# Performance work log

Hardware: AMD Instinct MI355X
Metric: run time of the kernel (lower is better)

Reference implementation:

```python
import jax, jax.numpy as jnp
import numpy as np

EMBED_DIM = 1024
NUM_HEADS = 16
HEAD_DIM = EMBED_DIM // NUM_HEADS
BSZ, TGT, SRC = 4, 1024, 2048


def setup_inputs() -> dict:
    key = jax.random.key(0)
    ks = jax.random.split(key, 12)
    init = 1.0 / np.sqrt(EMBED_DIM)
    return {
        "hidden_states": jax.random.normal(ks[0], (BSZ, TGT, EMBED_DIM), jnp.float32),
        "key_value_states": jax.random.normal(ks[1], (BSZ, SRC, EMBED_DIM), jnp.float32),
        "bias": jax.random.normal(ks[2], (BSZ, NUM_HEADS, TGT, SRC), jnp.float32),
        "Wq": jax.random.normal(ks[3], (EMBED_DIM, EMBED_DIM), jnp.float32) * init,
        "bq": jax.random.normal(ks[4], (EMBED_DIM,), jnp.float32) * init,
        "Wk": jax.random.normal(ks[5], (EMBED_DIM, EMBED_DIM), jnp.float32) * init,
        "bk": jax.random.normal(ks[6], (EMBED_DIM,), jnp.float32) * init,
        "Wv": jax.random.normal(ks[7], (EMBED_DIM, EMBED_DIM), jnp.float32) * init,
        "bv": jax.random.normal(ks[8], (EMBED_DIM,), jnp.float32) * init,
        "Wo": jax.random.normal(ks[9], (EMBED_DIM, EMBED_DIM), jnp.float32) * init,
        "bo": jax.random.normal(ks[10], (EMBED_DIM,), jnp.float32) * init,
    }


def reference(hidden_states, key_value_states, bias, Wq, bq, Wk, bk, Wv, bv, Wo, bo):
    B, T, E = hidden_states.shape
    S = key_value_states.shape[1]
    H, hd = NUM_HEADS, HEAD_DIM
    scaling = hd ** (-0.5)
    # torch Linear: y = x @ W^T + b
    q = (hidden_states @ Wq.T + bq) * scaling            # [B,T,E]
    k = key_value_states @ Wk.T + bk                     # [B,S,E]
    v = key_value_states @ Wv.T + bv                     # [B,S,E]
    q = q.reshape(B, T, H, hd).transpose(0, 2, 1, 3)     # [B,H,T,hd]
    k = k.reshape(B, S, H, hd).transpose(0, 2, 1, 3)     # [B,H,S,hd]
    v = v.reshape(B, S, H, hd).transpose(0, 2, 1, 3)     # [B,H,S,hd]
    scores = jnp.einsum('bhtd,bhsd->bhts', q, k) + bias  # [B,H,T,S]
    probs = jax.nn.softmax(scores, axis=-1)
    attn = jnp.einsum('bhts,bhsd->bhtd', probs, v)       # [B,H,T,hd]
    # Faithful to the original: reshape (B*H, T, hd) -> (B, T, E) WITHOUT
    # transposing heads back (this is how the torch source does it).
    attn = attn.reshape(B, T, E)
    return attn @ Wo.T + bo
```

## Files before the change

kernel.cpp:

```cpp
#include <hip/hip_runtime.h>

#define DEVI __device__ __forceinline__

typedef __attribute__((ext_vector_type(4))) float f32x4;
typedef __attribute__((ext_vector_type(8))) short bf16x8;

DEVI unsigned short f2bf(float f) {
  unsigned int u = __builtin_bit_cast(unsigned int, f);
  u += 0x7FFFu + ((u >> 16) & 1u);
  return (unsigned short)(u >> 16);
}

DEVI void load_lds16(const void* g, void* l) {
  __builtin_amdgcn_global_load_lds(
      (__attribute__((address_space(1))) void*)g,
      (__attribute__((address_space(3))) void*)l,
      16, 0, 0);
}

DEVI int xcd_swz(int bid, int chunk) { return (bid & 7) * chunk + (bid >> 3); }

struct CvtArgs {
  const float* src[6];
  unsigned short* dst[6];
  int cum[6];
};

__global__ __launch_bounds__(256) void cvt_all(CvtArgs a, int total4) {
  int i = blockIdx.x * 256 + threadIdx.x;
  if (i >= total4) return;
  int s = 0;
#pragma unroll
  for (int k = 1; k < 6; ++k) s += (i >= a.cum[k]);
  const int j = i - a.cum[s];
  const f32x4 v = __builtin_nontemporal_load((const f32x4*)a.src[s] + j);
  ushort4 o;
  o.x = f2bf(v[0]); o.y = f2bf(v[1]); o.z = f2bf(v[2]); o.w = f2bf(v[3]);
  reinterpret_cast<ushort4*>(a.dst[s])[j] = o;
}

template<bool OUT_BF16>
DEVI void gemm_core(const unsigned short* __restrict__ A,
                    const unsigned short* __restrict__ W,
                    const float* __restrict__ bias,
                    void* __restrict__ out,
                    float scale, int log2R,
                    long sb, long st, long sh, long sd,
                    int bx, int by, bool vt)
{
  constexpr int K = 1024;
  __shared__ unsigned short smem[2 * 128 * 64];
  unsigned short* As = smem;
  unsigned short* Bs = smem + 8192;

  const int tid  = threadIdx.x;
  const int wid  = tid >> 6;
  const int lane = tid & 63;
  const int m0 = bx * 128;
  const int n0 = by * 128;
  const int wr = (wid >> 1) * 64;
  const int wc = (wid & 1) * 64;
  const int lg = lane >> 4;
  const int ll = lane & 15;

  f32x4 acc[4][4] = {};

  const char* Ab = (const char*)A + (long)m0 * K * 2;
  const char* Wb = (const char*)W + (long)n0 * K * 2;
  char* AsB = (char*)As;
  char* BsB = (char*)Bs;
  const long rowstride = (long)K * 2;

  for (int kt = 0; kt < K; kt += 64) {
#pragma unroll
    for (int j = 0; j < 4; ++j) {
      const int o    = (wid * 4 + j) * 1024 + lane * 16;
      const int row  = o >> 7;
      const int colb = o & 127;
      load_lds16(Ab + (long)row * rowstride + (long)kt * 2 + colb, AsB + (wid * 4 + j) * 1024);
      load_lds16(Wb + (long)row * rowstride + (long)kt * 2 + colb, BsB + (wid * 4 + j) * 1024);
    }
    __syncthreads();
#pragma unroll
    for (int ks = 0; ks < 2; ++ks) {
      bf16x8 af[4], bfr[4];
#pragma unroll
      for (int i = 0; i < 4; ++i) {
        af[i]  = *(const bf16x8*)&As[(wr + i * 16 + ll) * 64 + ks * 32 + lg * 8];
        bfr[i] = *(const bf16x8*)&Bs[(wc + i * 16 + ll) * 64 + ks * 32 + lg * 8];
      }
#pragma unroll
      for (int i = 0; i < 4; ++i)
#pragma unroll
        for (int j = 0; j < 4; ++j)
          acc[i][j] = __builtin_amdgcn_mfma_f32_16x16x32_bf16(af[i], bfr[j], acc[i][j], 0, 0, 0);
    }
    __syncthreads();
  }

  const int Rmask  = (1 << log2R) - 1;
  const int m_base = m0 + wr;
  const int b   = m_base >> log2R;
  const int tbs = m_base & Rmask;
  const int nn  = n0 + wc;
  float bj[4];
#pragma unroll
  for (int j = 0; j < 4; ++j) bj[j] = bias[nn + j * 16 + ll];

  if (OUT_BF16 && vt) {
    unsigned short* Tw = smem + wid * 2176;
#pragma unroll
    for (int h2 = 0; h2 < 2; ++h2) {
#pragma unroll
      for (int jj = 0; jj < 2; ++jj) {
        const int j = h2 * 2 + jj;
#pragma unroll
        for (int i = 0; i < 4; ++i)
#pragma unroll
          for (int r = 0; r < 4; ++r)
            Tw[(jj * 16 + ll) * 68 + i * 16 + lg * 4 + r] = f2bf((acc[i][j][r] + bj[j]) * scale);
      }
      asm volatile("s_waitcnt lgkmcnt(0)" ::: "memory");
#pragma unroll
      for (int k = 0; k < 8; ++k) {
        const int dloc = k * 4 + lg;
        const int t4   = ll * 4;
        const ushort4 vv = *(const ushort4*)&Tw[dloc * 68 + t4];
        const int n = nn + h2 * 32 + dloc;
        const int h = n >> 6, dd = n & 63;
        *(ushort4*)((unsigned short*)out + (long)b * sb + (long)h * sh + (long)dd * sd + tbs + t4) = vv;
      }
      if (h2 == 0) asm volatile("s_waitcnt lgkmcnt(0)" ::: "memory");
    }
    return;
  }

  if (OUT_BF16) {
    const int h = nn >> 6;
    unsigned short* ob = (unsigned short*)out + (long)b * sb + (long)h * sh;
    unsigned short* Tw = smem + wid * 2176;
#pragma unroll
    for (int p = 0; p < 2; ++p) {
#pragma unroll
      for (int i2 = 0; i2 < 2; ++i2) {
        const int i = p * 2 + i2;
#pragma unroll
        for (int j = 0; j < 4; ++j)
#pragma unroll
          for (int r = 0; r < 4; ++r)
            Tw[(i2 * 16 + lg * 4 + r) * 68 + j * 16 + ll] = f2bf((acc[i][j][r] + bj[j]) * scale);
      }
      asm volatile("s_waitcnt lgkmcnt(0)" ::: "memory");
#pragma unroll
      for (int k = 0; k < 8; ++k) {
        const int t_loc = k * 4 + lg;
        const int d4    = ll * 4;
        const ushort4 vv = *(const ushort4*)&Tw[t_loc * 68 + d4];
        *(ushort4*)(ob + (long)(tbs + p * 32 + t_loc) * st + d4) = vv;
      }
      if (p == 0) asm volatile("s_waitcnt lgkmcnt(0)" ::: "memory");
    }
    return;
  }

  {
    float* ob = (float*)out + (long)b * sb + nn;
    float* TwF = (float*)smem + wid * 1056;
#pragma unroll
    for (int i = 0; i < 4; ++i) {
#pragma unroll
      for (int j = 0; j < 4; ++j)
#pragma unroll
        for (int r = 0; r < 4; ++r)
          TwF[(lg * 4 + r) * 66 + j * 16 + ll] = acc[i][j][r] + bj[j];
      asm volatile("s_waitcnt lgkmcnt(0)" ::: "memory");
#pragma unroll
      for (int k = 0; k < 8; ++k) {
        const int t_loc = k * 2 + (lane >> 5);
        const int c2    = (lane & 31) * 2;
        const float2 v = *(const float2*)&TwF[t_loc * 66 + c2];
        *(float2*)(ob + (long)(tbs + i * 16 + t_loc) * st + c2) = v;
      }
      if (i < 3) asm volatile("s_waitcnt lgkmcnt(0)" ::: "memory");
    }
  }
}

struct GemmDesc {
  const unsigned short* A;
  const unsigned short* W;
  const float* bias;
  unsigned short* out;
  float scale;
  int log2R;
  long sb, st, sh, sd;
};

__global__ __launch_bounds__(256) void gemm_qkv(GemmDesc d0, GemmDesc d1, GemmDesc d2) {
  int bid = xcd_swz(blockIdx.x, 160);
  const GemmDesc* d;
  bool vt = false;
  if (bid < 256)      { d = &d0; }
  else if (bid < 768) { d = &d1; bid -= 256; }
  else                { d = &d2; bid -= 768; vt = true; }
  gemm_core<true>(d->A, d->W, d->bias, d->out, d->scale, d->log2R,
                  d->sb, d->st, d->sh, d->sd, bid >> 3, bid & 7, vt);
}

__global__ __launch_bounds__(256) void gemm_o(
    const unsigned short* __restrict__ A,
    const unsigned short* __restrict__ W,
    const float* __restrict__ bias,
    float* __restrict__ out,
    long sb, long st, long sh, long sd)
{
  const int bid = xcd_swz(blockIdx.x, 32);
  gemm_core<false>(A, W, bias, out, 1.0f, 10, sb, st, sh, sd, bid >> 3, bid & 7, false);
}

__global__ __launch_bounds__(256, 4) void attn_fused(
    const unsigned short* __restrict__ Qb,
    const unsigned short* __restrict__ Kb,
    const unsigned short* __restrict__ Vt,
    const float* __restrict__ bias,
    unsigned short* __restrict__ Ob)
{
  constexpr int T = 1024, S = 2048;
  __shared__ unsigned short Ks[64 * 72];
  __shared__ unsigned short Vs[64 * 72];
  __shared__ unsigned short Ps[4][16 * 72];

  const int tid = threadIdx.x;
  const int w = tid >> 6, lane = tid & 63;
  const int lg = lane >> 4, ll = lane & 15;

  const int wg = xcd_swz(blockIdx.x, 128);
  const int bh = wg >> 4;
  const int tt = wg & 15;
  const int t0 = tt * 64;
  const int trow = t0 + w * 16;

  bf16x8 qf[2];
#pragma unroll
  for (int ks = 0; ks < 2; ++ks)
    qf[ks] = *(const bf16x8*)(Qb + ((long)bh * T + trow + ll) * 64 + ks * 32 + lg * 8);

  f32x4 acc[4] = {};
  float m_run = -1e30f, l_run = 0.0f;

  const char* Kg = (const char*)(Kb + (long)bh * S * 64);
  const char* Vg = (const char*)(Vt + (long)bh * 64 * S);
  const float* biasg = bias + ((long)bh * T + t0) * S;
  const float* bias_row = biasg + (long)(w * 16 + ll) * S + lg * 4;

  for (int sc = 0; sc < S / 64; ++sc) {
    const float* bp = bias_row + sc * 64;
    f32x4 b4[4];
#pragma unroll
    for (int sf = 0; sf < 4; ++sf)
      b4[sf] = __builtin_nontemporal_load((const f32x4*)(bp + sf * 16));

#pragma unroll
    for (int r2 = 0; r2 < 2; ++r2) {
      const int o = (tid + r2 * 256) * 16;
      const int row = o >> 7, colb = o & 127;
      uint4 kd = *(const uint4*)(Kg + (long)(sc * 64 + row) * 128 + colb);
      *(uint4*)((char*)&Ks[0] + row * 144 + colb) = kd;
      uint4 vd = *(const uint4*)(Vg + (long)row * (S * 2) + sc * 128 + colb);
      *(uint4*)((char*)&Vs[0] + row * 144 + colb) = vd;
    }
    __syncthreads();

    f32x4 sv[4] = {};
#pragma unroll
    for (int ks = 0; ks < 2; ++ks) {
      bf16x8 kf[4];
#pragma unroll
      for (int sf = 0; sf < 4; ++sf)
        kf[sf] = *(const bf16x8*)((const char*)&Ks[0] + (sf * 16 + ll) * 144 + (ks * 32 + lg * 8) * 2);
#pragma unroll
      for (int sf = 0; sf < 4; ++sf)
        sv[sf] = __builtin_amdgcn_mfma_f32_16x16x32_bf16(kf[sf], qf[ks], sv[sf], 0, 0, 0);
    }

#pragma unroll
    for (int sf = 0; sf < 4; ++sf) {
      sv[sf][0] += b4[sf][0]; sv[sf][1] += b4[sf][1];
      sv[sf][2] += b4[sf][2]; sv[sf][3] += b4[sf][3];
    }

    float cm = sv[0][0];
#pragma unroll
    for (int sf = 0; sf < 4; ++sf)
#pragma unroll
      for (int r = 0; r < 4; ++r) cm = fmaxf(cm, sv[sf][r]);
    cm = fmaxf(cm, __shfl_xor(cm, 16));
    cm = fmaxf(cm, __shfl_xor(cm, 32));

    const float mnew = fmaxf(m_run, cm);
    const float alpha = __expf(m_run - mnew);
    float ps = 0.0f;
#pragma unroll
    for (int sf = 0; sf < 4; ++sf)
#pragma unroll
      for (int r = 0; r < 4; ++r) {
        const float p = __expf(sv[sf][r] - mnew);
        sv[sf][r] = p;
        ps += p;
      }
    ps += __shfl_xor(ps, 16);
    ps += __shfl_xor(ps, 32);
    l_run = l_run * alpha + ps;
    m_run = mnew;

    float ar[4];
#pragma unroll
    for (int r = 0; r < 4; ++r) ar[r] = __shfl(alpha, lg * 4 + r);
#pragma unroll
    for (int df = 0; df < 4; ++df)
#pragma unroll
      for (int r = 0; r < 4; ++r) acc[df][r] *= ar[r];

    unsigned short* Pw = &Ps[w][0];
#pragma unroll
    for (int sf = 0; sf < 4; ++sf) {
      ushort4 pw;
      pw.x = f2bf(sv[sf][0]); pw.y = f2bf(sv[sf][1]);
      pw.z = f2bf(sv[sf][2]); pw.w = f2bf(sv[sf][3]);
      *(ushort4*)&Pw[ll * 72 + sf * 16 + lg * 4] = pw;
    }
    asm volatile("s_waitcnt lgkmcnt(0)" ::: "memory");
    __builtin_amdgcn_sched_barrier(0);

#pragma unroll
    for (int ks = 0; ks < 2; ++ks) {
      bf16x8 pa = *(const bf16x8*)((const char*)Pw + ll * 144 + ks * 64 + lg * 16);
      bf16x8 vf[4];
#pragma unroll
      for (int df = 0; df < 4; ++df)
        vf[df] = *(const bf16x8*)((const char*)&Vs[0] + (df * 16 + ll) * 144 + (ks * 32 + lg * 8) * 2);
#pragma unroll
      for (int df = 0; df < 4; ++df)
        acc[df] = __builtin_amdgcn_mfma_f32_16x16x32_bf16(pa, vf[df], acc[df], 0, 0, 0);
    }
    __syncthreads();
  }

  const float inv = 1.0f / l_run;
  float ir[4];
#pragma unroll
  for (int r = 0; r < 4; ++r) ir[r] = __shfl(inv, lg * 4 + r);
#pragma unroll
  for (int df = 0; df < 4; ++df)
#pragma unroll
    for (int r = 0; r < 4; ++r) {
      const long oo = ((long)bh * T + trow + lg * 4 + r) * 64 + df * 16 + ll;
      Ob[oo] = f2bf(acc[df][r] * ir[r]);
    }
}

extern "C" void kernel_launch(void* const* d_in, const int* in_sizes, int n_in,
                              void* d_out, int out_size, void* d_ws, size_t ws_size,
                              hipStream_t stream) {
  constexpr int B = 4, T = 1024, S = 2048, E = 1024;
  const float* hs   = (const float*)d_in[0];
  const float* kv   = (const float*)d_in[1];
  const float* bias = (const float*)d_in[2];
  const float* Wq   = (const float*)d_in[3];
  const float* bq   = (const float*)d_in[4];
  const float* Wk   = (const float*)d_in[5];
  const float* bk   = (const float*)d_in[6];
  const float* Wv   = (const float*)d_in[7];
  const float* bv   = (const float*)d_in[8];
  const float* Wo   = (const float*)d_in[9];
  const float* bo   = (const float*)d_in[10];

  char* ws = (char*)d_ws;
  const size_t MB = 1024 * 1024;
  unsigned short* hs_bf = (unsigned short*)(ws);
  unsigned short* kv_bf = (unsigned short*)(ws + 8 * MB);
  unsigned short* wq_bf = (unsigned short*)(ws + 24 * MB);
  unsigned short* wk_bf = (unsigned short*)(ws + 26 * MB);
  unsigned short* wv_bf = (unsigned short*)(ws + 28 * MB);
  unsigned short* wo_bf = (unsigned short*)(ws + 30 * MB);
  unsigned short* q_buf = (unsigned short*)(ws + 32 * MB);
  unsigned short* k_buf = (unsigned short*)(ws + 40 * MB);
  unsigned short* v_buf = (unsigned short*)(ws + 56 * MB);
  unsigned short* a_buf = (unsigned short*)(ws + 72 * MB);

  CvtArgs ca;
  ca.src[0] = hs;  ca.dst[0] = hs_bf;
  ca.src[1] = kv;  ca.dst[1] = kv_bf;
  ca.src[2] = Wq;  ca.dst[2] = wq_bf;
  ca.src[3] = Wk;  ca.dst[3] = wk_bf;
  ca.src[4] = Wv;  ca.dst[4] = wv_bf;
  ca.src[5] = Wo;  ca.dst[5] = wo_bf;
  const int n4_hs = B * T * E / 4, n4_kv = B * S * E / 4, n4_w = E * E / 4;
  ca.cum[0] = 0;
  ca.cum[1] = n4_hs;
  ca.cum[2] = n4_hs + n4_kv;
  ca.cum[3] = n4_hs + n4_kv + n4_w;
  ca.cum[4] = n4_hs + n4_kv + 2 * n4_w;
  ca.cum[5] = n4_hs + n4_kv + 3 * n4_w;
  const int total4 = n4_hs + n4_kv + 4 * n4_w;
  cvt_all<<<dim3((total4 + 255) / 256), dim3(256), 0, stream>>>(ca, total4);

  GemmDesc dq{hs_bf, wq_bf, bq, q_buf, 0.125f, 10,
              (long)T * E, 64L, (long)T * 64, 1L};
  GemmDesc dk{kv_bf, wk_bf, bk, k_buf, 1.0f, 11,
              (long)S * E, 64L, (long)S * 64, 1L};
  GemmDesc dv{kv_bf, wv_bf, bv, v_buf, 1.0f, 11,
              (long)S * E, 1L, (long)S * 64, (long)S};
  gemm_qkv<<<dim3(1280), 256, 0, stream>>>(dq, dk, dv);

  attn_fused<<<dim3(1024), 256, 0, stream>>>(q_buf, k_buf, v_buf, bias, a_buf);

  gemm_o<<<dim3(256), 256, 0, stream>>>(
      a_buf, wo_bf, bo, (float*)d_out,
      (long)T * E, (long)E, 64L, 1L);
}
```

Before: 277.3 us.

## Double query rows per wave in attention and prefetch K/V into registers

```diff
diff --git a/kernel.cpp b/kernel.cpp
--- a/kernel.cpp
+++ b/kernel.cpp
@@ -218,7 +218,7 @@
   gemm_core<false>(A, W, bias, out, 1.0f, 10, sb, st, sh, sd, bid >> 3, bid & 7, false);
 }
 
-__global__ __launch_bounds__(256, 4) void attn_fused(
+__global__ __launch_bounds__(256, 2) void attn_fused(
     const unsigned short* __restrict__ Qb,
     const unsigned short* __restrict__ Kb,
     const unsigned short* __restrict__ Vt,
@@ -228,50 +228,64 @@
   constexpr int T = 1024, S = 2048;
   __shared__ unsigned short Ks[64 * 72];
   __shared__ unsigned short Vs[64 * 72];
-  __shared__ unsigned short Ps[4][16 * 72];
+  __shared__ unsigned short Ps[4][32 * 72];
 
   const int tid = threadIdx.x;
   const int w = tid >> 6, lane = tid & 63;
   const int lg = lane >> 4, ll = lane & 15;
 
-  const int wg = xcd_swz(blockIdx.x, 128);
-  const int bh = wg >> 4;
-  const int tt = wg & 15;
-  const int t0 = tt * 64;
-  const int trow = t0 + w * 16;
-
-  bf16x8 qf[2];
-#pragma unroll
-  for (int ks = 0; ks < 2; ++ks)
-    qf[ks] = *(const bf16x8*)(Qb + ((long)bh * T + trow + ll) * 64 + ks * 32 + lg * 8);
-
-  f32x4 acc[4] = {};
-  float m_run = -1e30f, l_run = 0.0f;
+  const int wg = xcd_swz(blockIdx.x, 64);
+  const int bh = wg >> 3;
+  const int tt = wg & 7;
+  const int t0 = tt * 128;
+  const int trow = t0 + w * 32;
+
+  bf16x8 qf[2][2];
+#pragma unroll
+  for (int rf = 0; rf < 2; ++rf)
+#pragma unroll
+    for (int ks = 0; ks < 2; ++ks)
+      qf[rf][ks] = *(const bf16x8*)(Qb + ((long)bh * T + trow + rf * 16 + ll) * 64 + ks * 32 + lg * 8);
+
+  f32x4 acc[2][4] = {};
+  float m_run[2] = {-1e30f, -1e30f};
+  float l_run[2] = {0.0f, 0.0f};
 
   const char* Kg = (const char*)(Kb + (long)bh * S * 64);
   const char* Vg = (const char*)(Vt + (long)bh * 64 * S);
-  const float* biasg = bias + ((long)bh * T + t0) * S;
-  const float* bias_row = biasg + (long)(w * 16 + ll) * S + lg * 4;
+  const float* bias_base = bias + ((long)bh * T + trow + ll) * S + lg * 4;
+
+  const int o0 = tid * 16;
+  const int row0 = o0 >> 7, colb0 = o0 & 127;
+  const int o1 = (tid + 256) * 16;
+  const int row1 = o1 >> 7, colb1 = o1 & 127;
+  uint4 kreg[2], vreg[2];
+  auto load_chunk = [&](int sc) {
+    kreg[0] = *(const uint4*)(Kg + (long)(sc * 64 + row0) * 128 + colb0);
+    vreg[0] = *(const uint4*)(Vg + (long)row0 * (S * 2) + sc * 128 + colb0);
+    kreg[1] = *(const uint4*)(Kg + (long)(sc * 64 + row1) * 128 + colb1);
+    vreg[1] = *(const uint4*)(Vg + (long)row1 * (S * 2) + sc * 128 + colb1);
+  };
+  load_chunk(0);
 
   for (int sc = 0; sc < S / 64; ++sc) {
-    const float* bp = bias_row + sc * 64;
-    f32x4 b4[4];
-#pragma unroll
-    for (int sf = 0; sf < 4; ++sf)
-      b4[sf] = __builtin_nontemporal_load((const f32x4*)(bp + sf * 16));
-
-#pragma unroll
-    for (int r2 = 0; r2 < 2; ++r2) {
-      const int o = (tid + r2 * 256) * 16;
-      const int row = o >> 7, colb = o & 127;
-      uint4 kd = *(const uint4*)(Kg + (long)(sc * 64 + row) * 128 + colb);
-      *(uint4*)((char*)&Ks[0] + row * 144 + colb) = kd;
-      uint4 vd = *(const uint4*)(Vg + (long)row * (S * 2) + sc * 128 + colb);
-      *(uint4*)((char*)&Vs[0] + row * 144 + colb) = vd;
-    }
+    const float* bp = bias_base + sc * 64;
+    f32x4 b4[2][4];
+#pragma unroll
+    for (int rf = 0; rf < 2; ++rf)
+#pragma unroll
+      for (int sf = 0; sf < 4; ++sf)
+        b4[rf][sf] = __builtin_nontemporal_load((const f32x4*)(bp + (long)(rf * 16) * S + sf * 16));
+
+    *(uint4*)((char*)&Ks[0] + row0 * 144 + colb0) = kreg[0];
+    *(uint4*)((char*)&Vs[0] + row0 * 144 + colb0) = vreg[0];
+    *(uint4*)((char*)&Ks[0] + row1 * 144 + colb1) = kreg[1];
+    *(uint4*)((char*)&Vs[0] + row1 * 144 + colb1) = vreg[1];
+
+    if (sc + 1 < S / 64) load_chunk(sc + 1);
     __syncthreads();
 
-    f32x4 sv[4] = {};
+    f32x4 sv[2][4] = {};
 #pragma unroll
     for (int ks = 0; ks < 2; ++ks) {
       bf16x8 kf[4];
@@ -279,84 +293,95 @@
       for (int sf = 0; sf < 4; ++sf)
         kf[sf] = *(const bf16x8*)((const char*)&Ks[0] + (sf * 16 + ll) * 144 + (ks * 32 + lg * 8) * 2);
 #pragma unroll
+      for (int rf = 0; rf < 2; ++rf)
+#pragma unroll
+        for (int sf = 0; sf < 4; ++sf)
+          sv[rf][sf] = __builtin_amdgcn_mfma_f32_16x16x32_bf16(kf[sf], qf[rf][ks], sv[rf][sf], 0, 0, 0);
+    }
+
+    unsigned short* Pw = &Ps[w][0];
+#pragma unroll
+    for (int rf = 0; rf < 2; ++rf) {
+#pragma unroll
+      for (int sf = 0; sf < 4; ++sf) {
+        sv[rf][sf][0] += b4[rf][sf][0]; sv[rf][sf][1] += b4[rf][sf][1];
+        sv[rf][sf][2] += b4[rf][sf][2]; sv[rf][sf][3] += b4[rf][sf][3];
+      }
+      float cm = sv[rf][0][0];
+#pragma unroll
       for (int sf = 0; sf < 4; ++sf)
-        sv[sf] = __builtin_amdgcn_mfma_f32_16x16x32_bf16(kf[sf], qf[ks], sv[sf], 0, 0, 0);
-    }
-
-#pragma unroll
-    for (int sf = 0; sf < 4; ++sf) {
-      sv[sf][0] += b4[sf][0]; sv[sf][1] += b4[sf][1];
-      sv[sf][2] += b4[sf][2]; sv[sf][3] += b4[sf][3];
-    }
-
-    float cm = sv[0][0];
-#pragma unroll
-    for (int sf = 0; sf < 4; ++sf)
-#pragma unroll
-      for (int r = 0; r < 4; ++r) cm = fmaxf(cm, sv[sf][r]);
-    cm = fmaxf(cm, __shfl_xor(cm, 16));
-    cm = fmaxf(cm, __shfl_xor(cm, 32));
-
-    const float mnew = fmaxf(m_run, cm);
-    const float alpha = __expf(m_run - mnew);
-    float ps = 0.0f;
-#pragma unroll
-    for (int sf = 0; sf < 4; ++sf)
-#pragma unroll
-      for (int r = 0; r < 4; ++r) {
-        const float p = __expf(sv[sf][r] - mnew);
-        sv[sf][r] = p;
-        ps += p;
-      }
-    ps += __shfl_xor(ps, 16);
-    ps += __shfl_xor(ps, 32);
-    l_run = l_run * alpha + ps;
-    m_run = mnew;
-
-    float ar[4];
-#pragma unroll
-    for (int r = 0; r < 4; ++r) ar[r] = __shfl(alpha, lg * 4 + r);
-#pragma unroll
-    for (int df = 0; df < 4; ++df)
-#pragma unroll
-      for (int r = 0; r < 4; ++r) acc[df][r] *= ar[r];
-
-    unsigned short* Pw = &Ps[w][0];
-#pragma unroll
-    for (int sf = 0; sf < 4; ++sf) {
-      ushort4 pw;
-      pw.x = f2bf(sv[sf][0]); pw.y = f2bf(sv[sf][1]);
-      pw.z = f2bf(sv[sf][2]); pw.w = f2bf(sv[sf][3]);
-      *(ushort4*)&Pw[ll * 72 + sf * 16 + lg * 4] = pw;
+#pragma unroll
+        for (int r = 0; r < 4; ++r) cm = fmaxf(cm, sv[rf][sf][r]);
+      cm = fmaxf(cm, __shfl_xor(cm, 16));
+      cm = fmaxf(cm, __shfl_xor(cm, 32));
+
+      const float mnew = fmaxf(m_run[rf], cm);
+      const float alpha = __expf(m_run[rf] - mnew);
+      float ps = 0.0f;
+#pragma unroll
+      for (int sf = 0; sf < 4; ++sf)
+#pragma unroll
+        for (int r = 0; r < 4; ++r) {
+          const float p = __expf(sv[rf][sf][r] - mnew);
+          sv[rf][sf][r] = p;
+          ps += p;
+        }
+      ps += __shfl_xor(ps, 16);
+      ps += __shfl_xor(ps, 32);
+      l_run[rf] = l_run[rf] * alpha + ps;
+      m_run[rf] = mnew;
+
+      float ar[4];
+#pragma unroll
+      for (int r = 0; r < 4; ++r) ar[r] = __shfl(alpha, lg * 4 + r);
+#pragma unroll
+      for (int df = 0; df < 4; ++df)
+#pragma unroll
+        for (int r = 0; r < 4; ++r) acc[rf][df][r] *= ar[r];
+
+#pragma unroll
+      for (int sf = 0; sf < 4; ++sf) {
+        ushort4 pw;
+        pw.x = f2bf(sv[rf][sf][0]); pw.y = f2bf(sv[rf][sf][1]);
+        pw.z = f2bf(sv[rf][sf][2]); pw.w = f2bf(sv[rf][sf][3]);
+        *(ushort4*)&Pw[(rf * 16 + ll) * 72 + sf * 16 + lg * 4] = pw;
+      }
     }
     asm volatile("s_waitcnt lgkmcnt(0)" ::: "memory");
     __builtin_amdgcn_sched_barrier(0);
 
 #pragma unroll
     for (int ks = 0; ks < 2; ++ks) {
-      bf16x8 pa = *(const bf16x8*)((const char*)Pw + ll * 144 + ks * 64 + lg * 16);
-      bf16x8 vf[4];
+      bf16x8 pa[2], vf[4];
+#pragma unroll
+      for (int rf = 0; rf < 2; ++rf)
+        pa[rf] = *(const bf16x8*)((const char*)Pw + (rf * 16 + ll) * 144 + ks * 64 + lg * 16);
 #pragma unroll
       for (int df = 0; df < 4; ++df)
         vf[df] = *(const bf16x8*)((const char*)&Vs[0] + (df * 16 + ll) * 144 + (ks * 32 + lg * 8) * 2);
 #pragma unroll
-      for (int df = 0; df < 4; ++df)
-        acc[df] = __builtin_amdgcn_mfma_f32_16x16x32_bf16(pa, vf[df], acc[df], 0, 0, 0);
+      for (int rf = 0; rf < 2; ++rf)
+#pragma unroll
+        for (int df = 0; df < 4; ++df)
+          acc[rf][df] = __builtin_amdgcn_mfma_f32_16x16x32_bf16(pa[rf], vf[df], acc[rf][df], 0, 0, 0);
     }
     __syncthreads();
   }
 
-  const float inv = 1.0f / l_run;
-  float ir[4];
-#pragma unroll
-  for (int r = 0; r < 4; ++r) ir[r] = __shfl(inv, lg * 4 + r);
-#pragma unroll
-  for (int df = 0; df < 4; ++df)
-#pragma unroll
-    for (int r = 0; r < 4; ++r) {
-      const long oo = ((long)bh * T + trow + lg * 4 + r) * 64 + df * 16 + ll;
-      Ob[oo] = f2bf(acc[df][r] * ir[r]);
-    }
+#pragma unroll
+  for (int rf = 0; rf < 2; ++rf) {
+    const float inv = 1.0f / l_run[rf];
+    float ir[4];
+#pragma unroll
+    for (int r = 0; r < 4; ++r) ir[r] = __shfl(inv, lg * 4 + r);
+#pragma unroll
+    for (int df = 0; df < 4; ++df)
+#pragma unroll
+      for (int r = 0; r < 4; ++r) {
+        const long oo = ((long)bh * T + trow + rf * 16 + lg * 4 + r) * 64 + df * 16 + ll;
+        Ob[oo] = f2bf(acc[rf][df][r] * ir[r]);
+      }
+  }
 }
 
 extern "C" void kernel_launch(void* const* d_in, const int* in_sizes, int n_in,
@@ -413,7 +438,7 @@
               (long)S * E, 1L, (long)S * 64, (long)S};
   gemm_qkv<<<dim3(1280), 256, 0, stream>>>(dq, dk, dv);
 
-  attn_fused<<<dim3(1024), 256, 0, stream>>>(q_buf, k_buf, v_buf, bias, a_buf);
+  attn_fused<<<dim3(512), 256, 0, stream>>>(q_buf, k_buf, v_buf, bias, a_buf);
 
   gemm_o<<<dim3(256), 256, 0, stream>>>(
       a_buf, wo_bf, bo, (float*)d_out,
```

Result: slower. 323.7 us (+16.8%).
